# Optimization experiments

Measured on AMD Instinct MI355X. Metric: run time of the kernel, lower is better.

The kernel has to match this reference:

```python
import jax, jax.numpy as jnp
import numpy as np

N = 100000       # nodes
E = 1600000      # edges (avg degree 16)
D = 8            # node feat dim per layer (feat_dims=[8,8,8])
SE = 2           # static edge feats
EF = SE + 1 + D  # static + euclidian norm + direction vector = 11
NLAYERS = 2
EPS_BN = 1e-5
EPS_NORM = 1e-12
LRELU_SLOPE = 0.01


def setup_inputs() -> dict:
    key = jax.random.key(0)
    ks = jax.random.split(key, 3 + 6 * NLAYERS)
    inp = {
        "v": jax.random.normal(ks[0], (N, D), jnp.float32),
        "edge_index": jax.random.randint(ks[1], (2, E), 0, N, dtype=jnp.int64),
        "edge_attr": jax.random.uniform(ks[2], (E, SE), jnp.float32),
    }
    for l in range(NLAYERS):
        kk = ks[3 + 6 * l: 3 + 6 * (l + 1)]
        inp[f"en_w{l}"] = jax.random.normal(kk[0], (EF, D * D), jnp.float32) * 0.1
        inp[f"en_b{l}"] = jnp.zeros((D * D,), jnp.float32)
        inp[f"en_g{l}"] = jnp.ones((D * D,), jnp.float32)
        inp[f"en_beta{l}"] = jnp.zeros((D * D,), jnp.float32)
        inp[f"root_w{l}"] = jax.random.normal(kk[1], (D, D), jnp.float32) * 0.1
        inp[f"root_b{l}"] = jnp.zeros((D,), jnp.float32)
    return inp


def _edge_feat(vres, edge_attr, src, dst):
    # gather endpoints, L2-normalize difference, concat [static | norm | direction]
    d = vres[dst] - vres[src]                       # [E, D]
    n = jnp.linalg.norm(d, axis=1, keepdims=True)   # [E, 1]
    dirv = d / (n + EPS_NORM)                       # [E, D]
    return jnp.concatenate([edge_attr[:, :SE], n, dirv], axis=1)  # [E, EF]


def _gnn_layer(x, e, src, dst, en_w, en_b, en_g, en_beta, root_w, root_b):
    # edge_net: Linear -> BatchNorm1d (training stats) -> Tanh
    h = e @ en_w + en_b                             # [E, D*D]
    mu = jnp.mean(h, axis=0)
    var = jnp.var(h, axis=0)
    h = (h - mu) * jax.lax.rsqrt(var + EPS_BN) * en_g + en_beta
    w = jnp.tanh(h).reshape(-1, D, D)               # [E, D, D]
    # gather-matmul-scatter (NNConv-style, mean aggregation at dst)
    msg = jnp.einsum('ei,eio->eo', x[src], w)       # [E, D]
    agg = jax.ops.segment_sum(msg, dst, num_segments=N)
    cnt = jax.ops.segment_sum(jnp.ones((msg.shape[0], 1), msg.dtype), dst,
                              num_segments=N)
    agg = agg / jnp.maximum(cnt, 1.0)
    out = agg + x @ root_w + root_b                 # root_weight=True
    return jax.nn.leaky_relu(out, LRELU_SLOPE)      # act=True


def reference(v, edge_index, edge_attr,
              en_w0, en_b0, en_g0, en_beta0, root_w0, root_b0,
              en_w1, en_b1, en_g1, en_beta1, root_w1, root_b1):
    src, dst = edge_index[0], edge_index[1]
    vres = v
    layer_params = [
        (en_w0, en_b0, en_g0, en_beta0, root_w0, root_b0),
        (en_w1, en_b1, en_g1, en_beta1, root_w1, root_b1),
    ]
    for p in layer_params:  # dynamic_efeats='skip': edge feats from vres each layer
        e = _edge_feat(vres, edge_attr, src, dst)
        v = _gnn_layer(v, e, src, dst, *p)
    return v + vres  # residual=True
```

## Files before the change

kernel.cpp:

```cpp
#include <hip/hip_runtime.h>
#include <hip/hip_fp16.h>
#include <math.h>

#define NN 100000
#define NE 1600000
#define EPS_BN 1e-5f
#define EPS_NORM 1e-12f
#define SLOPE 0.01f
#define EXP_BLOCKS 1024
#define PART_BLOCKS 1024
#define NBUCK 391
#define NBLK 1563
#define CNT_LEN (NBUCK * NBLK)
#define CSB ((CNT_LEN + 255) / 256)
#define GS_LEN (64 * NBUCK)
#define GS_BLOCKS ((GS_LEN + 255) / 256)

typedef _Float16 h2 __attribute__((ext_vector_type(2)));

#if __has_builtin(__builtin_amdgcn_exp2f)
#define EXP2F(x) __builtin_amdgcn_exp2f(x)
#else
#define EXP2F(x) exp2f(x)
#endif

__device__ __forceinline__ float fast_tanh(float x) {
    float t = EXP2F(x * 2.885390082f);
    return fmaf(-2.0f, __builtin_amdgcn_rcpf(t + 1.0f), 1.0f);
}

__device__ __forceinline__ unsigned pk2(float a, float b) {
    union { __half2 h; unsigned u; } c;
    c.h = __float22half2_rn(make_float2(a, b));
    return c.u;
}

__device__ __forceinline__ h2 u2h(unsigned x) {
    union { unsigned u; h2 h; } c; c.u = x; return c.h;
}

#if __has_builtin(__builtin_amdgcn_fdot2)
#define FDOT2(A, B, C) __builtin_amdgcn_fdot2((A), (B), (C), false)
#else
__device__ __forceinline__ float FDOT2(h2 a, h2 b, float c) {
    return fmaf((float)a.x, (float)b.x, fmaf((float)a.y, (float)b.y, c));
}
#endif

__global__ void __launch_bounds__(256) r1_count_kernel(
    const int* __restrict__ ei, int* __restrict__ cntT)
{
    __shared__ int h[NBUCK];
    int b = blockIdx.x, t = threadIdx.x;
    for (int j = t; j < NBUCK; j += 256) h[j] = 0;
    __syncthreads();
    int e4 = b * 1024 + t * 4;
    if (e4 < NE) {
        int4 d4 = *(const int4*)(ei + NE + e4);
        atomicAdd(&h[d4.x >> 8], 1);
        atomicAdd(&h[d4.y >> 8], 1);
        atomicAdd(&h[d4.z >> 8], 1);
        atomicAdd(&h[d4.w >> 8], 1);
    }
    __syncthreads();
    for (int j = t; j < NBUCK; j += 256) cntT[(size_t)j * NBLK + b] = h[j];
}

__global__ void __launch_bounds__(256) gscanA_kernel(
    int* __restrict__ a, int* __restrict__ bs, int len)
{
    int b = blockIdx.x, t = threadIdx.x;
    int i = b * 256 + t;
    int d = (i < len) ? a[i] : 0;
    __shared__ int sh[256];
    sh[t] = d;
    __syncthreads();
    for (int off = 1; off < 256; off <<= 1) {
        int val = (t >= off) ? sh[t - off] : 0;
        __syncthreads();
        sh[t] += val;
        __syncthreads();
    }
    if (i < len) a[i] = sh[t] - d;
    if (t == 255) bs[b] = sh[255];
}

__global__ void __launch_bounds__(256) gscanB_kernel(
    int* __restrict__ a, const int* __restrict__ bs, int len)
{
    int b = blockIdx.x, t = threadIdx.x;
    __shared__ int sh[256];
    int s = 0;
    for (int j = t; j < b; j += 256) s += bs[j];
    sh[t] = s;
    __syncthreads();
    for (int off = 128; off > 0; off >>= 1) {
        if (t < off) sh[t] += sh[t + off];
        __syncthreads();
    }
    int boff = sh[0];
    int i = b * 256 + t;
    if (i < len) a[i] += boff;
}

__global__ void __launch_bounds__(256) r2_scatter_kernel(
    const int* __restrict__ ei, const float* __restrict__ ea,
    const int* __restrict__ cntT, unsigned long long* __restrict__ bucketed)
{
    __shared__ int h[NBUCK];
    __shared__ int base[NBUCK];
    int b = blockIdx.x, t = threadIdx.x;
    for (int j = t; j < NBUCK; j += 256) {
        h[j] = 0;
        base[j] = cntT[(size_t)j * NBLK + b];
    }
    __syncthreads();
    int e4 = b * 1024 + t * 4;
    if (e4 < NE) {
        int4 s4 = *(const int4*)(ei + e4);
        int4 d4 = *(const int4*)(ei + NE + e4);
        float4 a01 = *(const float4*)(ea + 2 * (size_t)e4);
        float4 a23 = *(const float4*)(ea + 2 * (size_t)e4 + 4);
#define DO_EDGE(S, D, A0, A1)                                                \
        {                                                                    \
            unsigned a0q = __float2uint_rn((A0) * 32768.0f);                 \
            if (a0q > 32767u) a0q = 32767u;                                  \
            unsigned a1q = __float2uint_rn((A1) * 32768.0f);                 \
            if (a1q > 32767u) a1q = 32767u;                                  \
            unsigned long long rec =                                         \
                  (((unsigned long long)(unsigned)(D)) << 47)                \
                | (((unsigned long long)(unsigned)(S)) << 30)                \
                | (((unsigned long long)a0q) << 15)                          \
                | ((unsigned long long)a1q);                                 \
            int bb = (D) >> 8;                                               \
            int lr = atomicAdd(&h[bb], 1);                                   \
            bucketed[base[bb] + lr] = rec;                                   \
        }
        DO_EDGE(s4.x, d4.x, a01.x, a01.y)
        DO_EDGE(s4.y, d4.y, a01.z, a01.w)
        DO_EDGE(s4.z, d4.z, a23.x, a23.y)
        DO_EDGE(s4.w, d4.w, a23.z, a23.w)
#undef DO_EDGE
    }
}

__global__ void __launch_bounds__(256) finalize_kernel(
    const unsigned long long* __restrict__ bucketed,
    const int* __restrict__ cntT,
    unsigned long long* __restrict__ recs8,
    int* __restrict__ rowptr, int* __restrict__ pr, int* __restrict__ bhT)
{
    __shared__ int hist[256], lps[256], lh[64];
    __shared__ unsigned short pos16[6144];
    int b = blockIdx.x, t = threadIdx.x;
    hist[t] = 0;
    if (t < 64) lh[t] = 0;
    __syncthreads();
    int bstart = cntT[(size_t)b * NBLK];
    int bend = (b == NBUCK - 1) ? NE : cntT[(size_t)(b + 1) * NBLK];

    for (int j = bstart + t; j < bend; j += 256) {
        unsigned long long r = bucketed[j];
        int dl = (int)((r >> 47) & 255u);
        int lr = atomicAdd(&hist[dl], 1);
        int o = j - bstart;
        if (o < 6144) pos16[o] = (unsigned short)lr;
    }
    __syncthreads();
    int d = hist[t];
    lps[t] = d;
    __syncthreads();
    for (int off = 1; off < 256; off <<= 1) {
        int val = (t >= off) ? lps[t - off] : 0;
        __syncthreads();
        lps[t] += val;
        __syncthreads();
    }
    int excl = lps[t] - d;
    int node = b * 256 + t;
    if (node < NN) {
        rowptr[node] = bstart + excl;
        int db = d < 63 ? d : 63;
        int bkt = 63 - db;
        int lr2 = atomicAdd(&lh[bkt], 1);
        pr[node] = (lr2 << 6) | bkt;
    }
    if (b == 0 && t == 0) rowptr[NN] = NE;
    __syncthreads();
    if (t < 64) bhT[t * NBUCK + b] = lh[t];
    for (int j = bstart + t; j < bend; j += 256) {
        unsigned long long r = bucketed[j];
        int dl = (int)((r >> 47) & 255u);
        int o = j - bstart;
        int lr = (o < 6144) ? (int)pos16[o] : 0;
        recs8[bstart + (lps[dl] - hist[dl]) + lr] = r;
    }
}

__global__ void __launch_bounds__(256, 4) expand_stats_kernel(
    const float* __restrict__ v,
    const unsigned long long* __restrict__ recs8,
    uint4* __restrict__ A16, uint2* __restrict__ B8,
    float* __restrict__ partials)
{
    float acc[39];
#pragma unroll
    for (int i = 0; i < 39; ++i) acc[i] = 0.0f;

    int tid = blockIdx.x * 256 + threadIdx.x;
    int hi = tid & 1;
    for (int eidx = tid >> 1; eidx < NE; eidx += (EXP_BLOCKS * 256) / 2) {
        unsigned long long r = recs8[eidx];
        int d = (int)(r >> 47);
        int s = (int)((r >> 30) & 0x1FFFFu);
        float a0 = (float)(unsigned)((r >> 15) & 0x7FFFu) * (1.0f / 32768.0f);
        float a1 = (float)(unsigned)(r & 0x7FFFu) * (1.0f / 32768.0f);

        float4 s0 = *(const float4*)(v + (size_t)s * 8);
        float4 s1 = *(const float4*)(v + (size_t)s * 8 + 4);
        float4 d0 = *(const float4*)(v + (size_t)d * 8);
        float4 d1 = *(const float4*)(v + (size_t)d * 8 + 4);
        float df[8];
        df[0] = d0.x - s0.x; df[1] = d0.y - s0.y;
        df[2] = d0.z - s0.z; df[3] = d0.w - s0.w;
        df[4] = d1.x - s1.x; df[5] = d1.y - s1.y;
        df[6] = d1.z - s1.z; df[7] = d1.w - s1.w;
        float nsq = 0.0f;
#pragma unroll
        for (int q = 0; q < 8; ++q) nsq = fmaf(df[q], df[q], nsq);
        float nrm = sqrtf(nsq);
        float inv = __builtin_amdgcn_rcpf(nrm + EPS_NORM);
        float e[11];
        e[0] = a0; e[1] = a1; e[2] = nrm;
#pragma unroll
        for (int q = 0; q < 8; ++q) e[3 + q] = df[q] * inv;

        if (!hi) {
#pragma unroll
            for (int k = 0; k < 11; ++k) acc[k] += e[k];
            int p = 11;
#pragma unroll
            for (int k = 0; k < 11; ++k)
#pragma unroll
                for (int l = k; l < 11; ++l) {
                    if (p < 39) acc[p] = fmaf(e[k], e[l], acc[p]);
                    ++p;
                }
            uint4 lo;
            lo.x = pk2(e[0], e[1]); lo.y = pk2(e[2], e[3]);
            lo.z = pk2(e[4], e[5]); lo.w = pk2(e[6], e[7]);
            A16[eidx] = lo;
        } else {
            int p = 11;
#pragma unroll
            for (int k = 0; k < 11; ++k)
#pragma unroll
                for (int l = k; l < 11; ++l) {
                    if (p >= 39) acc[p - 39] = fmaf(e[k], e[l], acc[p - 39]);
                    ++p;
                }
            unsigned q10 = __float2uint_rn((e[10] + 1.0f) * 16383.5f);
            if (q10 > 32767u) q10 = 32767u;
            uint2 hv;
            hv.x = pk2(e[8], e[9]);
            hv.y = ((unsigned)s << 15) | q10;
            B8[eidx] = hv;
        }
    }

#pragma unroll
    for (int i = 0; i < 39; ++i) {
        float x = acc[i];
        x += __shfl_down(x, 2);
        x += __shfl_down(x, 4);
        x += __shfl_down(x, 8);
        x += __shfl_down(x, 16);
        x += __shfl_down(x, 32);
        acc[i] = x;
    }
    __shared__ float lsum[4][77];
    int wave = threadIdx.x >> 6;
    int lane = threadIdx.x & 63;
    if (lane == 0) {
#pragma unroll
        for (int i = 0; i < 39; ++i) lsum[wave][i] = acc[i];
    }
    if (lane == 1) {
#pragma unroll
        for (int i = 0; i < 38; ++i) lsum[wave][39 + i] = acc[i];
    }
    __syncthreads();
    if (threadIdx.x < 77) {
        float t = lsum[0][threadIdx.x] + lsum[1][threadIdx.x]
                + lsum[2][threadIdx.x] + lsum[3][threadIdx.x];
        partials[blockIdx.x * 77 + threadIdx.x] = t;
    }
}

__global__ void bn_finalize_kernel(
    const float* __restrict__ partials,
    const float* __restrict__ w0, const float* __restrict__ b0,
    const float* __restrict__ g0, const float* __restrict__ be0,
    const float* __restrict__ w1, const float* __restrict__ b1,
    const float* __restrict__ g1, const float* __restrict__ be1,
    float* __restrict__ wbp)
{
    __shared__ double gs[77];
    int t = threadIdx.x;
    if (t < 77) {
        double s = 0.0;
        for (int b = 0; b < PART_BLOCKS; b += 4) {
            s += (double)partials[b * 77 + t] + (double)partials[(b + 1) * 77 + t]
               + (double)partials[(b + 2) * 77 + t] + (double)partials[(b + 3) * 77 + t];
        }
        gs[t] = s;
    }
    __syncthreads();
    if (t >= 128) return;
    int layer = t >> 6;
    int c = t & 63;
    const float* W  = layer ? w1 : w0;
    const float* B  = layer ? b1 : b0;
    const float* G  = layer ? g1 : g0;
    const float* BE = layer ? be1 : be0;

    const double invE = 1.0 / (double)NE;
    double m[11], wv[11];
    for (int k = 0; k < 11; ++k) {
        m[k] = gs[k] * invE;
        wv[k] = (double)W[k * 64 + c];
    }
    double md = 0.0;
    for (int k = 0; k < 11; ++k) md += m[k] * wv[k];
    double s2 = 0.0;
    int p = 11;
    for (int k = 0; k < 11; ++k)
        for (int l = k; l < 11; ++l) {
            double Me = gs[p] * invE; ++p;
            double term = Me * wv[k] * wv[l];
            s2 += (k == l) ? term : 2.0 * term;
        }
    double var = s2 - md * md;
    double mu = md + (double)B[c];
    float scale = (float)((double)G[c] / sqrt(var + (double)EPS_BN));
    float shift = (float)((double)BE[c] - mu * (double)scale);

    float* wpd = wbp + layer * 1152;
    for (int k = 0; k < 11; ++k) wpd[k * 64 + c] = W[k * 64 + c] * scale;
    wpd[704 + c] = fmaf(B[c], scale, shift);
    unsigned* pw = (unsigned*)(wpd + 768);
    for (int kp = 0; kp < 5; ++kp) {
        float wlo = W[(2 * kp) * 64 + c] * scale;
        float whi = W[(2 * kp + 1) * 64 + c] * scale;
        pw[kp * 64 + c] = pk2(wlo, whi);
    }
}

__global__ void __launch_bounds__(256) permB_kernel(
    const int* __restrict__ pr, const int* __restrict__ bhT,
    const int* __restrict__ rowptr, int4* __restrict__ perm4)
{
    int n = blockIdx.x * 256 + threadIdx.x;
    if (n >= NN) return;
    int p = pr[n];
    int bkt = p & 63, lrank = p >> 6, b = n >> 8;
    int pos = bhT[bkt * NBUCK + b] + lrank;
    perm4[pos] = make_int4(n, rowptr[n], rowptr[n + 1], 0);
}

#define FAT_BODY3(LO, HB, E10, XI)                                           \
    do {                                                                     \
        h2 ep0 = u2h((LO).x), ep1 = u2h((LO).y);                             \
        h2 ep2 = u2h((LO).z), ep3 = u2h((LO).w);                             \
        h2 ep4 = u2h((HB).x);                                                \
        _Pragma("unroll")                                                    \
        for (int o = 0; o < 8; ++o) {                                        \
            float hh = breg[o];                                              \
            hh = FDOT2(ep0, pw[0][o], hh);                                   \
            hh = FDOT2(ep1, pw[1][o], hh);                                   \
            hh = FDOT2(ep2, pw[2][o], hh);                                   \
            hh = FDOT2(ep3, pw[3][o], hh);                                   \
            hh = FDOT2(ep4, pw[4][o], hh);                                   \
            hh = fmaf((E10), w10[o], hh);                                    \
            msg[o] = fmaf((XI), fast_tanh(hh), msg[o]);                      \
        }                                                                    \
    } while (0)

template<int LAYER>
__global__ void __launch_bounds__(256)
__attribute__((amdgpu_waves_per_eu(2, 4))) layer_fat_kernel(
    const float* __restrict__ vres,
    const float* __restrict__ x,
    const uint4* __restrict__ A16, const uint2* __restrict__ B8,
    const int4* __restrict__ perm4,
    const float* __restrict__ wb,
    const float* __restrict__ rw, const float* __restrict__ rb,
    float* __restrict__ out)
{
    int g = blockIdx.x * 256 + threadIdx.x;
    int4 pm = perm4[g >> 3];
    int n = pm.x, rp0 = pm.y, rp1 = pm.z;
    int i = g & 7;

    h2 pw[5][8];
    const unsigned* pwg = (const unsigned*)(wb + 768);
#pragma unroll
    for (int kp = 0; kp < 5; ++kp) {
        uint4 pa = *(const uint4*)(pwg + kp * 64 + i * 8);
        uint4 pb = *(const uint4*)(pwg + kp * 64 + i * 8 + 4);
        pw[kp][0] = u2h(pa.x); pw[kp][1] = u2h(pa.y);
        pw[kp][2] = u2h(pa.z); pw[kp][3] = u2h(pa.w);
        pw[kp][4] = u2h(pb.x); pw[kp][5] = u2h(pb.y);
        pw[kp][6] = u2h(pb.z); pw[kp][7] = u2h(pb.w);
    }
    float w10[8];
    {
        float4 wa = *(const float4*)(wb + 640 + i * 8);
        float4 wc = *(const float4*)(wb + 640 + i * 8 + 4);
        w10[0] = wa.x; w10[1] = wa.y; w10[2] = wa.z; w10[3] = wa.w;
        w10[4] = wc.x; w10[5] = wc.y; w10[6] = wc.z; w10[7] = wc.w;
    }
    float breg[8];
    {
        float4 ba = *(const float4*)(wb + 704 + i * 8);
        float4 bb = *(const float4*)(wb + 704 + i * 8 + 4);
        breg[0] = ba.x; breg[1] = ba.y; breg[2] = ba.z; breg[3] = ba.w;
        breg[4] = bb.x; breg[5] = bb.y; breg[6] = bb.z; breg[7] = bb.w;
    }

    float4 vd0 = *(const float4*)(vres + (size_t)n * 8);
    float4 vd1 = *(const float4*)(vres + (size_t)n * 8 + 4);
    float vd[8] = {vd0.x, vd0.y, vd0.z, vd0.w, vd1.x, vd1.y, vd1.z, vd1.w};

    float msg[8];
#pragma unroll
    for (int o = 0; o < 8; ++o) msg[o] = 0.0f;

    int j = rp0;
    for (; j + 2 <= rp1; j += 2) {
        uint4 lo0 = A16[j];
        uint4 lo1 = A16[j + 1];
        uint2 hb0 = B8[j];
        uint2 hb1 = B8[j + 1];
        int s0 = (int)(hb0.y >> 15);
        int s1 = (int)(hb1.y >> 15);
        float e10a = fmaf((float)(hb0.y & 0x7FFFu), 1.0f / 16383.5f, -1.0f);
        float e10b = fmaf((float)(hb1.y & 0x7FFFu), 1.0f / 16383.5f, -1.0f);
        float xi0 = x[(size_t)s0 * 8 + i];
        float xi1 = x[(size_t)s1 * 8 + i];
        FAT_BODY3(lo0, hb0, e10a, xi0);
        FAT_BODY3(lo1, hb1, e10b, xi1);
    }
    if (j < rp1) {
        uint4 lo0 = A16[j];
        uint2 hb0 = B8[j];
        int s0 = (int)(hb0.y >> 15);
        float e10a = fmaf((float)(hb0.y & 0x7FFFu), 1.0f / 16383.5f, -1.0f);
        float xi0 = x[(size_t)s0 * 8 + i];
        FAT_BODY3(lo0, hb0, e10a, xi0);
    }

#pragma unroll
    for (int o = 0; o < 8; ++o) {
        float m = msg[o];
        m += __shfl_xor(m, 1);
        m += __shfl_xor(m, 2);
        m += __shfl_xor(m, 4);
        msg[o] = m;
    }
    float mo = msg[0];
#pragma unroll
    for (int o = 1; o < 8; ++o) if (i == o) mo = msg[o];

    float cf = (float)(rp1 - rp0);
    float invc = __builtin_amdgcn_rcpf(fmaxf(cf, 1.0f));

    float xn[8];
    if (LAYER == 0) {
#pragma unroll
        for (int q = 0; q < 8; ++q) xn[q] = vd[q];
    } else {
        float4 x0 = *(const float4*)(x + (size_t)n * 8);
        float4 x1 = *(const float4*)(x + (size_t)n * 8 + 4);
        xn[0] = x0.x; xn[1] = x0.y; xn[2] = x0.z; xn[3] = x0.w;
        xn[4] = x1.x; xn[5] = x1.y; xn[6] = x1.z; xn[7] = x1.w;
    }
    float a = fmaf(mo, invc, rb[i]);
#pragma unroll
    for (int k = 0; k < 8; ++k) a = fmaf(xn[k], rw[k * 8 + i], a);
    float y = (a > 0.0f) ? a : SLOPE * a;
    if (LAYER == 1) y += vres[(size_t)n * 8 + i];
    out[(size_t)n * 8 + i] = y;
}

extern "C" void kernel_launch(void* const* d_in, const int* in_sizes, int n_in,
                              void* d_out, int out_size, void* d_ws, size_t ws_size,
                              hipStream_t stream) {
    const float* v  = (const float*)d_in[0];
    const int* ei   = (const int*)d_in[1];
    const float* ea = (const float*)d_in[2];
    const float* en_w0  = (const float*)d_in[3];
    const float* en_b0  = (const float*)d_in[4];
    const float* en_g0  = (const float*)d_in[5];
    const float* en_be0 = (const float*)d_in[6];
    const float* rw0    = (const float*)d_in[7];
    const float* rb0    = (const float*)d_in[8];
    const float* en_w1  = (const float*)d_in[9];
    const float* en_b1  = (const float*)d_in[10];
    const float* en_g1  = (const float*)d_in[11];
    const float* en_be1 = (const float*)d_in[12];
    const float* rw1    = (const float*)d_in[13];
    const float* rb1    = (const float*)d_in[14];

    char* ws = (char*)d_ws;
    float* partials = (float*)(ws);
    float* wbp      = (float*)(ws + 327680);
    int*   rowptr   = (int*)  (ws + 340992);
    int*   pr       = (int*)  (ws + 741376);
    int4*  perm4    = (int4*) (ws + 1141760);
    int*   bhT      = (int*)  (ws + 2741760);
    int*   gbsum    = (int*)  (ws + 2841856);
    int*   cbsum    = (int*)  (ws + 2842368);
    int*   cntT     = (int*)  (ws + 2852096);
    float* v1       = (float*)(ws + 5296640);
    unsigned long long* bucketed = (unsigned long long*)(ws + 8497152);
    uint4* A16      = (uint4*)(ws + 8497152);
    uint2* B8       = (uint2*)(ws + 34097152);
    unsigned long long* recs8 = (unsigned long long*)(ws + 46897152);
    float* vout     = (float*)d_out;

    r1_count_kernel<<<NBLK, 256, 0, stream>>>(ei, cntT);
    gscanA_kernel<<<CSB, 256, 0, stream>>>(cntT, cbsum, CNT_LEN);
    gscanB_kernel<<<CSB, 256, 0, stream>>>(cntT, cbsum, CNT_LEN);
    r2_scatter_kernel<<<NBLK, 256, 0, stream>>>(ei, ea, cntT, bucketed);
    finalize_kernel<<<NBUCK, 256, 0, stream>>>(bucketed, cntT, recs8, rowptr, pr, bhT);
    gscanA_kernel<<<GS_BLOCKS, 256, 0, stream>>>(bhT, gbsum, GS_LEN);
    gscanB_kernel<<<GS_BLOCKS, 256, 0, stream>>>(bhT, gbsum, GS_LEN);
    permB_kernel<<<NBUCK, 256, 0, stream>>>(pr, bhT, rowptr, perm4);
    expand_stats_kernel<<<EXP_BLOCKS, 256, 0, stream>>>(v, recs8, A16, B8, partials);
    bn_finalize_kernel<<<1, 128, 0, stream>>>(partials, en_w0, en_b0, en_g0, en_be0,
                                              en_w1, en_b1, en_g1, en_be1, wbp);

    const int LB = (NN * 8) / 256;
    layer_fat_kernel<0><<<LB, 256, 0, stream>>>(v, v,  A16, B8, perm4, wbp,        rw0, rb0, v1);
    layer_fat_kernel<1><<<LB, 256, 0, stream>>>(v, v1, A16, B8, perm4, wbp + 1152, rw1, rb1, vout);
}
```

Baseline: 209.5 us.

## Fuse edge expansion and BN statistics into CSR finalize kernel

The separate expand_stats kernel is folded into finalize_kernel. Each bucket block now computes the edge features directly from its bucketed records and writes A16/B8 at their sorted positions, which removes the recs8 intermediate buffer, one kernel launch, and a full pass over the edge records. Finalize moves to 512 threads, and adjacent lanes swap their edge features with shuffles so the moment accumulation stays split across lane pairs. The trade-offs are that only 391 blocks now carry the heavy per-edge work, the writes become scattered, and the layer kernel's waves_per_eu bound is also changed.

```diff
diff --git a/kernel.cpp b/kernel.cpp
--- a/kernel.cpp
+++ b/kernel.cpp
@@ -7,8 +7,6 @@
 #define EPS_BN 1e-5f
 #define EPS_NORM 1e-12f
 #define SLOPE 0.01f
-#define EXP_BLOCKS 1024
-#define PART_BLOCKS 1024
 #define NBUCK 391
 #define NBLK 1563
 #define CNT_LEN (NBUCK * NBLK)
@@ -144,22 +142,25 @@
     }
 }
 
-__global__ void __launch_bounds__(256) finalize_kernel(
+__global__ void __launch_bounds__(512) finalize_kernel(
     const unsigned long long* __restrict__ bucketed,
     const int* __restrict__ cntT,
-    unsigned long long* __restrict__ recs8,
-    int* __restrict__ rowptr, int* __restrict__ pr, int* __restrict__ bhT)
+    const float* __restrict__ v,
+    uint4* __restrict__ A16, uint2* __restrict__ B8,
+    int* __restrict__ rowptr, int* __restrict__ pr, int* __restrict__ bhT,
+    float* __restrict__ partials)
 {
     __shared__ int hist[256], lps[256], lh[64];
     __shared__ unsigned short pos16[6144];
+    __shared__ float lsum[8][77];
     int b = blockIdx.x, t = threadIdx.x;
-    hist[t] = 0;
+    if (t < 256) hist[t] = 0;
     if (t < 64) lh[t] = 0;
     __syncthreads();
     int bstart = cntT[(size_t)b * NBLK];
     int bend = (b == NBUCK - 1) ? NE : cntT[(size_t)(b + 1) * NBLK];
 
-    for (int j = bstart + t; j < bend; j += 256) {
+    for (int j = bstart + t; j < bend; j += 512) {
         unsigned long long r = bucketed[j];
         int dl = (int)((r >> 47) & 255u);
         int lr = atomicAdd(&hist[dl], 1);
@@ -167,19 +168,18 @@
         if (o < 6144) pos16[o] = (unsigned short)lr;
     }
     __syncthreads();
-    int d = hist[t];
-    lps[t] = d;
+    int d = (t < 256) ? hist[t] : 0;
+    if (t < 256) lps[t] = d;
     __syncthreads();
     for (int off = 1; off < 256; off <<= 1) {
-        int val = (t >= off) ? lps[t - off] : 0;
+        int val = (t >= off && t < 256) ? lps[t - off] : 0;
         __syncthreads();
-        lps[t] += val;
+        if (t < 256) lps[t] += val;
         __syncthreads();
     }
-    int excl = lps[t] - d;
     int node = b * 256 + t;
-    if (node < NN) {
-        rowptr[node] = bstart + excl;
+    if (t < 256 && node < NN) {
+        rowptr[node] = bstart + lps[t] - d;
         int db = d < 63 ? d : 63;
         int bkt = 63 - db;
         int lr2 = atomicAdd(&lh[bkt], 1);
@@ -188,83 +188,85 @@
     if (b == 0 && t == 0) rowptr[NN] = NE;
     __syncthreads();
     if (t < 64) bhT[t * NBUCK + b] = lh[t];
-    for (int j = bstart + t; j < bend; j += 256) {
-        unsigned long long r = bucketed[j];
-        int dl = (int)((r >> 47) & 255u);
-        int o = j - bstart;
-        int lr = (o < 6144) ? (int)pos16[o] : 0;
-        recs8[bstart + (lps[dl] - hist[dl]) + lr] = r;
-    }
-}
-
-__global__ void __launch_bounds__(256, 4) expand_stats_kernel(
-    const float* __restrict__ v,
-    const unsigned long long* __restrict__ recs8,
-    uint4* __restrict__ A16, uint2* __restrict__ B8,
-    float* __restrict__ partials)
-{
+
     float acc[39];
 #pragma unroll
     for (int i = 0; i < 39; ++i) acc[i] = 0.0f;
 
-    int tid = blockIdx.x * 256 + threadIdx.x;
-    int hi = tid & 1;
-    for (int eidx = tid >> 1; eidx < NE; eidx += (EXP_BLOCKS * 256) / 2) {
-        unsigned long long r = recs8[eidx];
-        int d = (int)(r >> 47);
-        int s = (int)((r >> 30) & 0x1FFFFu);
-        float a0 = (float)(unsigned)((r >> 15) & 0x7FFFu) * (1.0f / 32768.0f);
-        float a1 = (float)(unsigned)(r & 0x7FFFu) * (1.0f / 32768.0f);
-
-        float4 s0 = *(const float4*)(v + (size_t)s * 8);
-        float4 s1 = *(const float4*)(v + (size_t)s * 8 + 4);
-        float4 d0 = *(const float4*)(v + (size_t)d * 8);
-        float4 d1 = *(const float4*)(v + (size_t)d * 8 + 4);
-        float df[8];
-        df[0] = d0.x - s0.x; df[1] = d0.y - s0.y;
-        df[2] = d0.z - s0.z; df[3] = d0.w - s0.w;
-        df[4] = d1.x - s1.x; df[5] = d1.y - s1.y;
-        df[6] = d1.z - s1.z; df[7] = d1.w - s1.w;
-        float nsq = 0.0f;
-#pragma unroll
-        for (int q = 0; q < 8; ++q) nsq = fmaf(df[q], df[q], nsq);
-        float nrm = sqrtf(nsq);
-        float inv = __builtin_amdgcn_rcpf(nrm + EPS_NORM);
+    for (int j = bstart + t; (j - (t & 1)) < bend; j += 512) {
+        bool valid = j < bend;
         float e[11];
-        e[0] = a0; e[1] = a1; e[2] = nrm;
-#pragma unroll
-        for (int q = 0; q < 8; ++q) e[3 + q] = df[q] * inv;
-
-        if (!hi) {
-#pragma unroll
-            for (int k = 0; k < 11; ++k) acc[k] += e[k];
-            int p = 11;
-#pragma unroll
-            for (int k = 0; k < 11; ++k)
-#pragma unroll
-                for (int l = k; l < 11; ++l) {
-                    if (p < 39) acc[p] = fmaf(e[k], e[l], acc[p]);
-                    ++p;
-                }
+        if (valid) {
+            unsigned long long r = bucketed[j];
+            int dl = (int)((r >> 47) & 255u);
+            int s = (int)((r >> 30) & 0x1FFFFu);
+            float a0 = (float)(unsigned)((r >> 15) & 0x7FFFu) * (1.0f / 32768.0f);
+            float a1 = (float)(unsigned)(r & 0x7FFFu) * (1.0f / 32768.0f);
+            int dn = b * 256 + dl;
+            float4 s0 = *(const float4*)(v + (size_t)s * 8);
+            float4 s1 = *(const float4*)(v + (size_t)s * 8 + 4);
+            float4 d0 = *(const float4*)(v + (size_t)dn * 8);
+            float4 d1 = *(const float4*)(v + (size_t)dn * 8 + 4);
+            float df[8];
+            df[0] = d0.x - s0.x; df[1] = d0.y - s0.y;
+            df[2] = d0.z - s0.z; df[3] = d0.w - s0.w;
+            df[4] = d1.x - s1.x; df[5] = d1.y - s1.y;
+            df[6] = d1.z - s1.z; df[7] = d1.w - s1.w;
+            float nsq = 0.0f;
+#pragma unroll
+            for (int q = 0; q < 8; ++q) nsq = fmaf(df[q], df[q], nsq);
+            float nrm = sqrtf(nsq);
+            float inv = __builtin_amdgcn_rcpf(nrm + EPS_NORM);
+            e[0] = a0; e[1] = a1; e[2] = nrm;
+#pragma unroll
+            for (int q = 0; q < 8; ++q) e[3 + q] = df[q] * inv;
+
+            int o = j - bstart;
+            int lr = (o < 6144) ? (int)pos16[o] : 0;
+            int pos = bstart + (lps[dl] - hist[dl]) + lr;
             uint4 lo;
             lo.x = pk2(e[0], e[1]); lo.y = pk2(e[2], e[3]);
             lo.z = pk2(e[4], e[5]); lo.w = pk2(e[6], e[7]);
-            A16[eidx] = lo;
-        } else {
-            int p = 11;
-#pragma unroll
-            for (int k = 0; k < 11; ++k)
-#pragma unroll
-                for (int l = k; l < 11; ++l) {
-                    if (p >= 39) acc[p - 39] = fmaf(e[k], e[l], acc[p - 39]);
-                    ++p;
-                }
+            A16[pos] = lo;
             unsigned q10 = __float2uint_rn((e[10] + 1.0f) * 16383.5f);
             if (q10 > 32767u) q10 = 32767u;
             uint2 hv;
             hv.x = pk2(e[8], e[9]);
             hv.y = ((unsigned)s << 15) | q10;
-            B8[eidx] = hv;
+            B8[pos] = hv;
+        } else {
+#pragma unroll
+            for (int k = 0; k < 11; ++k) e[k] = 0.0f;
+        }
+        float eo[11];
+#pragma unroll
+        for (int k = 0; k < 11; ++k) eo[k] = __shfl_xor(e[k], 1);
+        if (!(t & 1)) {
+#pragma unroll
+            for (int k = 0; k < 11; ++k) acc[k] += e[k] + eo[k];
+            int p = 11;
+#pragma unroll
+            for (int k = 0; k < 11; ++k)
+#pragma unroll
+                for (int l = k; l < 11; ++l) {
+                    if (p < 39) {
+                        acc[p] = fmaf(e[k], e[l], acc[p]);
+                        acc[p] = fmaf(eo[k], eo[l], acc[p]);
+                    }
+                    ++p;
+                }
+        } else {
+            int p = 11;
+#pragma unroll
+            for (int k = 0; k < 11; ++k)
+#pragma unroll
+                for (int l = k; l < 11; ++l) {
+                    if (p >= 39) {
+                        acc[p - 39] = fmaf(e[k], e[l], acc[p - 39]);
+                        acc[p - 39] = fmaf(eo[k], eo[l], acc[p - 39]);
+                    }
+                    ++p;
+                }
         }
     }
 
@@ -278,9 +280,8 @@
         x += __shfl_down(x, 32);
         acc[i] = x;
     }
-    __shared__ float lsum[4][77];
-    int wave = threadIdx.x >> 6;
-    int lane = threadIdx.x & 63;
+    int wave = t >> 6;
+    int lane = t & 63;
     if (lane == 0) {
 #pragma unroll
         for (int i = 0; i < 39; ++i) lsum[wave][i] = acc[i];
@@ -290,10 +291,11 @@
         for (int i = 0; i < 38; ++i) lsum[wave][39 + i] = acc[i];
     }
     __syncthreads();
-    if (threadIdx.x < 77) {
-        float t = lsum[0][threadIdx.x] + lsum[1][threadIdx.x]
-                + lsum[2][threadIdx.x] + lsum[3][threadIdx.x];
-        partials[blockIdx.x * 77 + threadIdx.x] = t;
+    if (t < 77) {
+        float s = 0.0f;
+#pragma unroll
+        for (int w = 0; w < 8; ++w) s += lsum[w][t];
+        partials[b * 77 + t] = s;
     }
 }
 
@@ -309,10 +311,7 @@
     int t = threadIdx.x;
     if (t < 77) {
         double s = 0.0;
-        for (int b = 0; b < PART_BLOCKS; b += 4) {
-            s += (double)partials[b * 77 + t] + (double)partials[(b + 1) * 77 + t]
-               + (double)partials[(b + 2) * 77 + t] + (double)partials[(b + 3) * 77 + t];
-        }
+        for (int b = 0; b < NBUCK; ++b) s += (double)partials[b * 77 + t];
         gs[t] = s;
     }
     __syncthreads();
@@ -388,7 +387,7 @@
 
 template<int LAYER>
 __global__ void __launch_bounds__(256)
-__attribute__((amdgpu_waves_per_eu(2, 4))) layer_fat_kernel(
+__attribute__((amdgpu_waves_per_eu(2, 6))) layer_fat_kernel(
     const float* __restrict__ vres,
     const float* __restrict__ x,
     const uint4* __restrict__ A16, const uint2* __restrict__ B8,
@@ -514,30 +513,29 @@
 
     char* ws = (char*)d_ws;
     float* partials = (float*)(ws);
-    float* wbp      = (float*)(ws + 327680);
-    int*   rowptr   = (int*)  (ws + 340992);
-    int*   pr       = (int*)  (ws + 741376);
-    int4*  perm4    = (int4*) (ws + 1141760);
-    int*   bhT      = (int*)  (ws + 2741760);
-    int*   gbsum    = (int*)  (ws + 2841856);
-    int*   cbsum    = (int*)  (ws + 2842368);
-    int*   cntT     = (int*)  (ws + 2852096);
-    float* v1       = (float*)(ws + 5296640);
-    unsigned long long* bucketed = (unsigned long long*)(ws + 8497152);
-    uint4* A16      = (uint4*)(ws + 8497152);
-    uint2* B8       = (uint2*)(ws + 34097152);
-    unsigned long long* recs8 = (unsigned long long*)(ws + 46897152);
+    float* wbp      = (float*)(ws + 131072);
+    int*   rowptr   = (int*)  (ws + 143360);
+    int*   pr       = (int*)  (ws + 543744);
+    int4*  perm4    = (int4*) (ws + 944128);
+    int*   bhT      = (int*)  (ws + 2544128);
+    int*   gbsum    = (int*)  (ws + 2644224);
+    int*   cbsum    = (int*)  (ws + 2644736);
+    int*   cntT     = (int*)  (ws + 2654336);
+    float* v1       = (float*)(ws + 5099008);
+    unsigned long long* bucketed = (unsigned long long*)(ws + 8299520);
+    uint4* A16      = (uint4*)(ws + 21099520);
+    uint2* B8       = (uint2*)(ws + 46699520);
     float* vout     = (float*)d_out;
 
     r1_count_kernel<<<NBLK, 256, 0, stream>>>(ei, cntT);
     gscanA_kernel<<<CSB, 256, 0, stream>>>(cntT, cbsum, CNT_LEN);
     gscanB_kernel<<<CSB, 256, 0, stream>>>(cntT, cbsum, CNT_LEN);
     r2_scatter_kernel<<<NBLK, 256, 0, stream>>>(ei, ea, cntT, bucketed);
-    finalize_kernel<<<NBUCK, 256, 0, stream>>>(bucketed, cntT, recs8, rowptr, pr, bhT);
+    finalize_kernel<<<NBUCK, 512, 0, stream>>>(bucketed, cntT, v, A16, B8,
+                                               rowptr, pr, bhT, partials);
     gscanA_kernel<<<GS_BLOCKS, 256, 0, stream>>>(bhT, gbsum, GS_LEN);
     gscanB_kernel<<<GS_BLOCKS, 256, 0, stream>>>(bhT, gbsum, GS_LEN);
     permB_kernel<<<NBUCK, 256, 0, stream>>>(pr, bhT, rowptr, perm4);
-    expand_stats_kernel<<<EXP_BLOCKS, 256, 0, stream>>>(v, recs8, A16, B8, partials);
     bn_finalize_kernel<<<1, 128, 0, stream>>>(partials, en_w0, en_b0, en_g0, en_be0,
                                               en_w1, en_b1, en_g1, en_be1, wbp);
 
```

Measured after the change: 225.6 us. 7.7% more time.
